# Optimization experiments

Hardware: AMD Instinct MI355X
Metric: run time of the kernel (lower is better)

The kernel has to match this reference:

```python
import jax, jax.numpy as jnp
import numpy as np

ENT_TOTAL = 500000
REL_TOTAL = 1000
H = 128
B = 1024
K = 10  # negative_ent + negative_rel
MARGIN = 1.0


def setup_inputs() -> dict:
    key = jax.random.key(0)
    ks = jax.random.split(key, 8)
    return {
        "ent_embeddings": jax.random.normal(ks[0], (ENT_TOTAL, H), dtype=jnp.float32) * 0.05,
        "rel_matrices": jax.random.normal(ks[1], (REL_TOTAL, H * H), dtype=jnp.float32) * 0.05,
        "pos_h": jax.random.randint(ks[2], (B,), 0, ENT_TOTAL, dtype=jnp.int32),
        "pos_t": jax.random.randint(ks[3], (B,), 0, ENT_TOTAL, dtype=jnp.int32),
        "pos_r": jax.random.randint(ks[4], (B,), 0, REL_TOTAL, dtype=jnp.int32),
        "neg_h": jax.random.randint(ks[5], (B * K,), 0, ENT_TOTAL, dtype=jnp.int32),
        "neg_t": jax.random.randint(ks[6], (B * K,), 0, ENT_TOTAL, dtype=jnp.int32),
        "neg_r": jax.random.randint(ks[7], (B * K,), 0, REL_TOTAL, dtype=jnp.int32),
    }


def _calc_score(ent_emb, rel_mat, h_idx, t_idx, r_idx):
    # gather embeddings / relation matrices per example
    h = ent_emb[h_idx]                          # [N, H]
    t = ent_emb[t_idx]                          # [N, H]
    r = rel_mat[r_idx].reshape(-1, H, H)        # [N, H, H]
    # h * (r @ t), then sum over hidden dim -> per-example score [N]
    rt = jnp.einsum('nij,nj->ni', r, t)         # [N, H]
    return jnp.sum(h * rt, axis=-1)             # [N]


def reference(ent_embeddings, rel_matrices, pos_h, pos_t, pos_r, neg_h, neg_t, neg_r):
    p_score = _calc_score(ent_embeddings, rel_matrices, pos_h, pos_t, pos_r)  # [B]
    n_all = _calc_score(ent_embeddings, rel_matrices, neg_h, neg_t, neg_r)    # [B*K]
    # mean over the K negatives per positive (matches reduce_mean over axis 1)
    n_score = jnp.mean(n_all.reshape(B, K), axis=1)                           # [B]
    loss = jnp.sum(jnp.maximum(n_score - p_score + MARGIN, 0.0))
    return loss
```

## Files before the change

### kernel.cpp

```cpp
#include <hip/hip_runtime.h>

#define H 128
#define NPOS 1024
#define KNEG 10
#define NNEG (NPOS * KNEG)
#define NTOT (NPOS + NNEG)
#define NREL 1000
#define MAXL 256

__global__ __launch_bounds__(256) void rescal_rel_kernel(
    const float* __restrict__ ent,
    const float* __restrict__ rel,
    const int* __restrict__ pos_h, const int* __restrict__ pos_t,
    const int* __restrict__ pos_r,
    const int* __restrict__ neg_h, const int* __restrict__ neg_t,
    const int* __restrict__ neg_r,
    float* __restrict__ scores)
{
    const int r   = blockIdx.x;
    const int tid = threadIdx.x;

    __shared__ float sR[H * H];
    __shared__ float sht[4][4][H];
    __shared__ int   list[MAXL];
    __shared__ int   cnt;

    if (tid == 0) cnt = 0;
    __syncthreads();

    {
        const float4* __restrict__ Rg = (const float4*)(rel + (size_t)r * (H * H));
        float4* __restrict__ Rs = (float4*)sR;
#pragma unroll
        for (int m = 0; m < 16; ++m)
            Rs[m * 256 + tid] = Rg[m * 256 + tid];
    }

    {
        const int4* __restrict__ pr4 = (const int4*)pos_r;
        const int4* __restrict__ nr4 = (const int4*)neg_r;
        for (int q = tid; q < NTOT / 4; q += 256) {
            int4 v; int base;
            if (q < NPOS / 4) { v = pr4[q];            base = q * 4; }
            else              { v = nr4[q - NPOS / 4]; base = NPOS + (q - NPOS / 4) * 4; }
            if (v.x == r) { int p = atomicAdd(&cnt, 1); if (p < MAXL) list[p] = base + 0; }
            if (v.y == r) { int p = atomicAdd(&cnt, 1); if (p < MAXL) list[p] = base + 1; }
            if (v.z == r) { int p = atomicAdd(&cnt, 1); if (p < MAXL) list[p] = base + 2; }
            if (v.w == r) { int p = atomicAdd(&cnt, 1); if (p < MAXL) list[p] = base + 3; }
        }
    }
    __syncthreads();

    const int m    = cnt < MAXL ? cnt : MAXL;
    const int wave = tid >> 6;
    const int lane = tid & 63;
    const int half = lane >> 5;
    const int jcb  = lane & 31;

    float* __restrict__ h0s = sht[wave][0];
    float* __restrict__ t0s = sht[wave][1];
    float* __restrict__ h1s = sht[wave][2];
    float* __restrict__ t1s = sht[wave][3];

    auto fetch = [&](int i, float2& fh, float2& ft) {
        const int n  = list[i];
        const int hi = (n < NPOS) ? pos_h[n] : neg_h[n - NPOS];
        const int ti = (n < NPOS) ? pos_t[n] : neg_t[n - NPOS];
        fh = ((const float2*)(ent + (size_t)hi * H))[lane];
        ft = ((const float2*)(ent + (size_t)ti * H))[lane];
    };

    int p = wave;
    float2 ph0, pt0, ph1, pt1;
    if (2 * p < m) {
        fetch(2 * p, ph0, pt0);
        fetch((2 * p + 1 < m) ? 2 * p + 1 : 2 * p, ph1, pt1);
    }

    while (2 * p < m) {
        const int  n0   = list[2 * p];
        const bool has1 = (2 * p + 1 < m);
        const int  n1   = has1 ? list[2 * p + 1] : n0;

        ((float2*)h0s)[lane] = ph0;
        ((float2*)t0s)[lane] = pt0;
        ((float2*)h1s)[lane] = ph1;
        ((float2*)t1s)[lane] = pt1;
        asm volatile("s_waitcnt lgkmcnt(0)" ::: "memory");

        const int np = p + 4;
        if (2 * np < m) {
            fetch(2 * np, ph0, pt0);
            fetch((2 * np + 1 < m) ? 2 * np + 1 : 2 * np, ph1, pt1);
        }

        const float4  t04  = *(const float4*)&t0s[4 * jcb];
        const float4  t14  = *(const float4*)&t1s[4 * jcb];
        const float4* h04p = (const float4*)&h0s[half * 64];
        const float4* h14p = (const float4*)&h1s[half * 64];
        const float4* Rr4  = (const float4*)&sR[(size_t)half * 64 * H];

        float acc0 = 0.f, acc1 = 0.f;
#pragma unroll
        for (int kk = 0; kk < 16; ++kk) {
            const float4 h04 = h04p[kk];
            const float4 h14 = h14p[kk];
#pragma unroll
            for (int d = 0; d < 4; ++d) {
                const float4 r4 = Rr4[(kk * 4 + d) * 32 + jcb];
                const float dot0 = r4.x * t04.x + r4.y * t04.y + r4.z * t04.z + r4.w * t04.w;
                const float dot1 = r4.x * t14.x + r4.y * t14.y + r4.z * t14.z + r4.w * t14.w;
                const float h0v = (d == 0) ? h04.x : (d == 1) ? h04.y : (d == 2) ? h04.z : h04.w;
                const float h1v = (d == 0) ? h14.x : (d == 1) ? h14.y : (d == 2) ? h14.z : h14.w;
                acc0 += h0v * dot0;
                acc1 += h1v * dot1;
            }
        }

#pragma unroll
        for (int mask = 32; mask > 0; mask >>= 1) {
            acc0 += __shfl_xor(acc0, mask, 64);
            acc1 += __shfl_xor(acc1, mask, 64);
        }
        if (lane == 0) {
            scores[n0] = acc0;
            if (has1) scores[n1] = acc1;
        }
        p = np;
    }
}

__global__ __launch_bounds__(1024) void rescal_loss_kernel(
    const float* __restrict__ scores,
    float* __restrict__ out)
{
    const int b = threadIdx.x;
    const float p = scores[b];
    const float* __restrict__ neg = scores + NPOS + b * KNEG;
    float ns = 0.0f;
#pragma unroll
    for (int k = 0; k < KNEG; ++k) ns += neg[k];
    ns *= (1.0f / KNEG);

    float l = fmaxf(ns - p + 1.0f, 0.0f);

#pragma unroll
    for (int off = 32; off > 0; off >>= 1)
        l += __shfl_down(l, off, 64);

    __shared__ float red[16];
    const int wave = b >> 6;
    if ((b & 63) == 0) red[wave] = l;
    __syncthreads();
    if (b == 0) {
        float s = 0.0f;
#pragma unroll
        for (int w = 0; w < 16; ++w) s += red[w];
        out[0] = s;
    }
}

extern "C" void kernel_launch(void* const* d_in, const int* in_sizes, int n_in,
                              void* d_out, int out_size, void* d_ws, size_t ws_size,
                              hipStream_t stream) {
    const float* ent   = (const float*)d_in[0];
    const float* rel   = (const float*)d_in[1];
    const int* pos_h   = (const int*)d_in[2];
    const int* pos_t   = (const int*)d_in[3];
    const int* pos_r   = (const int*)d_in[4];
    const int* neg_h   = (const int*)d_in[5];
    const int* neg_t   = (const int*)d_in[6];
    const int* neg_r   = (const int*)d_in[7];

    float* scores = (float*)d_ws;
    float* out    = (float*)d_out;

    rescal_rel_kernel<<<NREL, 256, 0, stream>>>(
        ent, rel, pos_h, pos_t, pos_r, neg_h, neg_t, neg_r, scores);
    rescal_loss_kernel<<<1, 1024, 0, stream>>>(scores, out);
}
```

Baseline: 346.2 us.

## Split each relation matrix into four row blocks across separate workgroups

Each relation is now handled by four workgroups, each loading a quarter of the H×H matrix into LDS and computing partial scores over its 32 rows. The partial scores go to four separate workspace slices, and the loss kernel sums them. This cuts LDS per block from 64KB to about 16KB, which raises occupancy, and gives 4000 blocks instead of 1000. In exchange, every block repeats the scan of the index lists, and the t embeddings are gathered four times.

```diff
diff --git a/kernel.cpp b/kernel.cpp
--- a/kernel.cpp
+++ b/kernel.cpp
@@ -7,6 +7,8 @@
 #define NTOT (NPOS + NNEG)
 #define NREL 1000
 #define MAXL 256
+#define QSPLIT 4
+#define QROWS (H / QSPLIT)
 
 __global__ __launch_bounds__(256) void rescal_rel_kernel(
     const float* __restrict__ ent,
@@ -17,11 +19,13 @@
     const int* __restrict__ neg_r,
     float* __restrict__ scores)
 {
-    const int r   = blockIdx.x;
+    const int bid = blockIdx.x;
+    const int r   = bid >> 2;
+    const int q   = bid & 3;
     const int tid = threadIdx.x;
 
-    __shared__ float sR[H * H];
-    __shared__ float sht[4][4][H];
+    __shared__ float sR[QROWS * H];
+    __shared__ float sht[4][320];
     __shared__ int   list[MAXL];
     __shared__ int   cnt;
 
@@ -29,20 +33,21 @@
     __syncthreads();
 
     {
-        const float4* __restrict__ Rg = (const float4*)(rel + (size_t)r * (H * H));
+        const float4* __restrict__ Rg =
+            (const float4*)(rel + (size_t)r * (H * H) + (size_t)q * (QROWS * H));
         float4* __restrict__ Rs = (float4*)sR;
 #pragma unroll
-        for (int m = 0; m < 16; ++m)
-            Rs[m * 256 + tid] = Rg[m * 256 + tid];
+        for (int m4 = 0; m4 < 4; ++m4)
+            Rs[m4 * 256 + tid] = Rg[m4 * 256 + tid];
     }
 
     {
         const int4* __restrict__ pr4 = (const int4*)pos_r;
         const int4* __restrict__ nr4 = (const int4*)neg_r;
-        for (int q = tid; q < NTOT / 4; q += 256) {
+        for (int s = tid; s < NTOT / 4; s += 256) {
             int4 v; int base;
-            if (q < NPOS / 4) { v = pr4[q];            base = q * 4; }
-            else              { v = nr4[q - NPOS / 4]; base = NPOS + (q - NPOS / 4) * 4; }
+            if (s < NPOS / 4) { v = pr4[s];            base = s * 4; }
+            else              { v = nr4[s - NPOS / 4]; base = NPOS + (s - NPOS / 4) * 4; }
             if (v.x == r) { int p = atomicAdd(&cnt, 1); if (p < MAXL) list[p] = base + 0; }
             if (v.y == r) { int p = atomicAdd(&cnt, 1); if (p < MAXL) list[p] = base + 1; }
             if (v.z == r) { int p = atomicAdd(&cnt, 1); if (p < MAXL) list[p] = base + 2; }
@@ -57,16 +62,18 @@
     const int half = lane >> 5;
     const int jcb  = lane & 31;
 
-    float* __restrict__ h0s = sht[wave][0];
-    float* __restrict__ t0s = sht[wave][1];
-    float* __restrict__ h1s = sht[wave][2];
-    float* __restrict__ t1s = sht[wave][3];
+    float* __restrict__ hs0 = &sht[wave][0];
+    float* __restrict__ hs1 = &sht[wave][32];
+    float* __restrict__ ts0 = &sht[wave][64];
+    float* __restrict__ ts1 = &sht[wave][192];
+
+    float* __restrict__ sq = scores + (size_t)q * NTOT;
 
     auto fetch = [&](int i, float2& fh, float2& ft) {
         const int n  = list[i];
         const int hi = (n < NPOS) ? pos_h[n] : neg_h[n - NPOS];
         const int ti = (n < NPOS) ? pos_t[n] : neg_t[n - NPOS];
-        fh = ((const float2*)(ent + (size_t)hi * H))[lane];
+        fh = ((const float2*)(ent + (size_t)hi * H + q * QROWS))[lane & 15];
         ft = ((const float2*)(ent + (size_t)ti * H))[lane];
     };
 
@@ -82,10 +89,12 @@
         const bool has1 = (2 * p + 1 < m);
         const int  n1   = has1 ? list[2 * p + 1] : n0;
 
-        ((float2*)h0s)[lane] = ph0;
-        ((float2*)t0s)[lane] = pt0;
-        ((float2*)h1s)[lane] = ph1;
-        ((float2*)t1s)[lane] = pt1;
+        ((float2*)ts0)[lane] = pt0;
+        ((float2*)ts1)[lane] = pt1;
+        if (lane < 16) {
+            ((float2*)hs0)[lane] = ph0;
+            ((float2*)hs1)[lane] = ph1;
+        }
         asm volatile("s_waitcnt lgkmcnt(0)" ::: "memory");
 
         const int np = p + 4;
@@ -94,17 +103,17 @@
             fetch((2 * np + 1 < m) ? 2 * np + 1 : 2 * np, ph1, pt1);
         }
 
-        const float4  t04  = *(const float4*)&t0s[4 * jcb];
-        const float4  t14  = *(const float4*)&t1s[4 * jcb];
-        const float4* h04p = (const float4*)&h0s[half * 64];
-        const float4* h14p = (const float4*)&h1s[half * 64];
-        const float4* Rr4  = (const float4*)&sR[(size_t)half * 64 * H];
+        const float4  t04 = *(const float4*)&ts0[4 * jcb];
+        const float4  t14 = *(const float4*)&ts1[4 * jcb];
+        const float4* h0p = (const float4*)&hs0[half * 16];
+        const float4* h1p = (const float4*)&hs1[half * 16];
+        const float4* Rr4 = (const float4*)&sR[(size_t)(half * 16) * H];
 
         float acc0 = 0.f, acc1 = 0.f;
 #pragma unroll
-        for (int kk = 0; kk < 16; ++kk) {
-            const float4 h04 = h04p[kk];
-            const float4 h14 = h14p[kk];
+        for (int kk = 0; kk < 4; ++kk) {
+            const float4 h04 = h0p[kk];
+            const float4 h14 = h1p[kk];
 #pragma unroll
             for (int d = 0; d < 4; ++d) {
                 const float4 r4 = Rr4[(kk * 4 + d) * 32 + jcb];
@@ -123,8 +132,8 @@
             acc1 += __shfl_xor(acc1, mask, 64);
         }
         if (lane == 0) {
-            scores[n0] = acc0;
-            if (has1) scores[n1] = acc1;
+            sq[n0] = acc0;
+            if (has1) sq[n1] = acc1;
         }
         p = np;
     }
@@ -135,11 +144,20 @@
     float* __restrict__ out)
 {
     const int b = threadIdx.x;
-    const float p = scores[b];
-    const float* __restrict__ neg = scores + NPOS + b * KNEG;
+
+    float p = 0.0f;
+#pragma unroll
+    for (int qq = 0; qq < QSPLIT; ++qq) p += scores[(size_t)qq * NTOT + b];
+
     float ns = 0.0f;
 #pragma unroll
-    for (int k = 0; k < KNEG; ++k) ns += neg[k];
+    for (int k = 0; k < KNEG; ++k) {
+        float s = 0.0f;
+#pragma unroll
+        for (int qq = 0; qq < QSPLIT; ++qq)
+            s += scores[(size_t)qq * NTOT + NPOS + b * KNEG + k];
+        ns += s;
+    }
     ns *= (1.0f / KNEG);
 
     float l = fmaxf(ns - p + 1.0f, 0.0f);
@@ -175,7 +193,7 @@
     float* scores = (float*)d_ws;
     float* out    = (float*)d_out;
 
-    rescal_rel_kernel<<<NREL, 256, 0, stream>>>(
+    rescal_rel_kernel<<<NREL * QSPLIT, 256, 0, stream>>>(
         ent, rel, pos_h, pos_t, pos_r, neg_h, neg_t, neg_r, scores);
     rescal_loss_kernel<<<1, 1024, 0, stream>>>(scores, out);
 }
```

Result: no change. 351.4 us (+1.5%).
